# Kernel optimization log

Hardware: AMD Instinct MI355X
Metric: run time of the kernel (lower is better)

Reference implementation:

```python
import jax, jax.numpy as jnp
import numpy as np

B, S, D, DFF = 4, 2048, 1024, 4096


def setup_inputs() -> dict:
    key = jax.random.key(0)
    ks = jax.random.split(key, 7)
    scale = 1.0 / np.sqrt(D)
    return {
        "x": jax.random.normal(ks[0], (B, S, D), dtype=jnp.float32),
        "wq": jax.random.normal(ks[1], (D, D), dtype=jnp.float32) * scale,
        "wk": jax.random.normal(ks[2], (D, D), dtype=jnp.float32) * scale,
        "wv": jax.random.normal(ks[3], (D, D), dtype=jnp.float32) * scale,
        "wo": jax.random.normal(ks[4], (D, D), dtype=jnp.float32) * scale,
        "w1": jax.random.normal(ks[5], (D, DFF), dtype=jnp.float32) * scale,
        "w2": jax.random.normal(ks[6], (DFF, D), dtype=jnp.float32) * (1.0 / np.sqrt(DFF)),
    }


def reference(x, wq, wk, wv, wo, w1, w2):
    # Single-head attention, NO 1/sqrt(d) scaling (faithful to source).
    q = x @ wq  # [B,S,D]
    k = x @ wk
    v = x @ wv
    scores = jnp.einsum("bsd,btd->bst", q, k)  # [B,S,S]
    weights = jax.nn.softmax(scores, axis=-1)
    attn = jnp.einsum("bst,btd->bsd", weights, v)
    proj = attn @ wo
    hidden = jax.nn.relu(proj @ w1)  # [B,S,DFF]
    out = hidden @ w2
    return out + x
```

## Files before the change

### kernel.cpp

```cpp
#include <hip/hip_runtime.h>
#include <hip/hip_bf16.h>
#include <hip/hip_fp16.h>


typedef _Float16 f16;
typedef __attribute__((ext_vector_type(8))) _Float16 f16x8;
typedef __attribute__((ext_vector_type(4))) _Float16 f16x4;
typedef __attribute__((ext_vector_type(4))) float f32x4;

#define BM 128
#define BN 128
#define BK 64

__device__ inline void gload16(const void* g, void* l) {
    __builtin_amdgcn_global_load_lds(
        (const __attribute__((address_space(1))) void*)g,
        (__attribute__((address_space(3))) void*)l, 16, 0, 0);
}

template<int EPI>
__global__ __launch_bounds__(256, 2)
void gemm_f16(const f16* __restrict__ A, const f16* __restrict__ Bt,
              const float* __restrict__ Res, void* __restrict__ Cv,
              int K, int lda, int ldb, int ldc,
              long long sA, long long sB, long long sC)
{
    __shared__ char smem[32 * 1024];
    f16* Ash = (f16*)smem;
    f16* Bsh = (f16*)(smem + 16384);
    float* xbuf = (float*)smem;

    const int t = threadIdx.x;
    const int z = blockIdx.z;
    A  += (size_t)z * sA;
    Bt += (size_t)z * sB;

    const int bm0 = blockIdx.x * BM;
    const int bn0 = blockIdx.y * BN;

    const int lane = t & 63;
    const int wid  = t >> 6;
    const int quad = lane >> 4;
    const int m16  = lane & 15;
    const int ks   = wid & 1;
    const int wn64 = (wid >> 1) * 64;

    const int r0 = t >> 3;
    const int kc = ((t & 7) ^ (r0 & 7)) * 8;
    const char* gA[4]; const char* gB[4];
    #pragma unroll
    for (int i = 0; i < 4; ++i) {
        gA[i] = (const char*)(A  + (size_t)(bm0 + i * 32 + r0) * lda + kc);
        gB[i] = (const char*)(Bt + (size_t)(bn0 + i * 32 + r0) * ldb + kc);
    }
    char* lA = (char*)Ash + (wid << 10);
    char* lB = (char*)Bsh + (wid << 10);

    f32x4 acc[8][4] = {};

    const int nk = K / BK;
    #define ISSUE(kt) do { const int ko = (kt) * 128;   \
        gload16(gA[0] + ko, lA);                        \
        gload16(gA[1] + ko, lA + 4096);                 \
        gload16(gA[2] + ko, lA + 8192);                 \
        gload16(gA[3] + ko, lA + 12288);                \
        gload16(gB[0] + ko, lB);                        \
        gload16(gB[1] + ko, lB + 4096);                 \
        gload16(gB[2] + ko, lB + 8192);                 \
        gload16(gB[3] + ko, lB + 12288); } while (0)

    const int swz = m16 & 7;
    const int ha  = ((ks * 4 + quad) ^ swz) * 8;

    ISSUE(0);
    for (int kt = 0; kt < nk; ++kt) {
        __syncthreads();
        f16x8 af[8], bf[4];
        #pragma unroll
        for (int i = 0; i < 8; ++i)
            af[i] = *(const f16x8*)&Ash[(i * 16 + m16) * BK + ha];
        #pragma unroll
        for (int j = 0; j < 4; ++j)
            bf[j] = *(const f16x8*)&Bsh[(wn64 + j * 16 + m16) * BK + ha];
        __syncthreads();
        if (kt + 1 < nk) ISSUE(kt + 1);
        #pragma unroll
        for (int i = 0; i < 8; ++i)
            #pragma unroll
            for (int j = 0; j < 4; ++j)
                acc[i][j] = __builtin_amdgcn_mfma_f32_16x16x32_f16(
                                af[i], bf[j], acc[i][j], 0, 0, 0);
    }
    #undef ISSUE

    float* xb = xbuf + (wid >> 1) * 4096;
    #define XIDX(row, col) ((row) * 64 + ((col) ^ (((row) & 4) << 2)))
    if (ks == 1) {
        #pragma unroll
        for (int i = 0; i < 4; ++i)
            #pragma unroll
            for (int j = 0; j < 4; ++j)
                #pragma unroll
                for (int ri = 0; ri < 4; ++ri)
                    xb[XIDX(i * 16 + quad * 4 + ri, j * 16 + m16)] = acc[i][j][ri];
    }
    __syncthreads();
    if (ks == 0) {
        #pragma unroll
        for (int i = 0; i < 4; ++i)
            #pragma unroll
            for (int j = 0; j < 4; ++j)
                #pragma unroll
                for (int ri = 0; ri < 4; ++ri)
                    acc[i][j][ri] += xb[XIDX(i * 16 + quad * 4 + ri, j * 16 + m16)];
    }
    __syncthreads();
    if (ks == 0) {
        #pragma unroll
        for (int i = 0; i < 4; ++i)
            #pragma unroll
            for (int j = 0; j < 4; ++j)
                #pragma unroll
                for (int ri = 0; ri < 4; ++ri)
                    xb[XIDX(i * 16 + quad * 4 + ri, j * 16 + m16)] = acc[i + 4][j][ri];
    }
    __syncthreads();
    if (ks == 1) {
        #pragma unroll
        for (int i = 0; i < 4; ++i)
            #pragma unroll
            for (int j = 0; j < 4; ++j)
                #pragma unroll
                for (int ri = 0; ri < 4; ++ri)
                    acc[i + 4][j][ri] += xb[XIDX(i * 16 + quad * 4 + ri, j * 16 + m16)];
    }
    #undef XIDX

    #define STORE_TILE(IB, RB)                                                  \
        do {                                                                    \
            if (EPI <= 1) {                                                     \
                f16* C = (f16*)Cv + (size_t)z * sC;                             \
                _Pragma("unroll")                                               \
                for (int i = 0; i < 4; ++i)                                     \
                    _Pragma("unroll")                                           \
                    for (int ri = 0; ri < 4; ++ri) {                            \
                        const size_t row = (size_t)(bm0 + (RB) + i * 16 + quad * 4 + ri); \
                        f16* cp = C + row * ldc + (bn0 + wn64 + m16);           \
                        _Pragma("unroll")                                       \
                        for (int j = 0; j < 4; ++j) {                           \
                            float v = acc[(IB) + i][j][ri];                     \
                            if (EPI == 1) v = fmaxf(v, 0.0f);                   \
                            cp[j * 16] = (f16)v;                                \
                        }                                                       \
                    }                                                           \
            } else {                                                            \
                float* C = (float*)Cv + (size_t)z * sC;                         \
                _Pragma("unroll")                                               \
                for (int i = 0; i < 4; ++i)                                     \
                    _Pragma("unroll")                                           \
                    for (int ri = 0; ri < 4; ++ri) {                            \
                        const size_t row = (size_t)(bm0 + (RB) + i * 16 + quad * 4 + ri); \
                        float* cp = C + row * ldc + (bn0 + wn64 + m16);         \
                        const float* rp = (EPI == 3)                            \
                            ? Res + row * ldc + (bn0 + wn64 + m16) : nullptr;   \
                        _Pragma("unroll")                                       \
                        for (int j = 0; j < 4; ++j) {                           \
                            float v = acc[(IB) + i][j][ri];                     \
                            if (EPI == 3) v += rp[j * 16];                      \
                            cp[j * 16] = v;                                     \
                        }                                                       \
                    }                                                           \
            }                                                                   \
        } while (0)

    if (ks == 0) STORE_TILE(0, 0);
    else         STORE_TILE(4, 64);
    #undef STORE_TILE
}

template<int EPI>
__global__ __launch_bounds__(256, 2)
void gemm_ns(const f16* __restrict__ A, const f16* __restrict__ Bt,
             void* __restrict__ Cv,
             int K, int lda, int ldb, int ldc)
{
    __shared__ f16 Ash[BM * BK];
    __shared__ f16 Bsh[BN * BK];

    const int t = threadIdx.x;
    const int bm0 = blockIdx.x * BM;
    const int bn0 = blockIdx.y * BN;

    const int lane = t & 63;
    const int wid  = t >> 6;
    const int quad = lane >> 4;
    const int m16  = lane & 15;
    const int wm = (wid & 1) * 64;
    const int wn = (wid >> 1) * 64;

    const int r0 = t >> 3;
    const int kc = ((t & 7) ^ (r0 & 7)) * 8;
    const char* gA[4]; const char* gB[4];
    #pragma unroll
    for (int i = 0; i < 4; ++i) {
        gA[i] = (const char*)(A  + (size_t)(bm0 + i * 32 + r0) * lda + kc);
        gB[i] = (const char*)(Bt + (size_t)(bn0 + i * 32 + r0) * ldb + kc);
    }
    char* lA = (char*)Ash + (wid << 10);
    char* lB = (char*)Bsh + (wid << 10);

    f32x4 acc[4][4] = {};

    const int nk = K / BK;
    #define ISSUE(kt) do { const int ko = (kt) * 128;   \
        gload16(gA[0] + ko, lA);                        \
        gload16(gA[1] + ko, lA + 4096);                 \
        gload16(gA[2] + ko, lA + 8192);                 \
        gload16(gA[3] + ko, lA + 12288);                \
        gload16(gB[0] + ko, lB);                        \
        gload16(gB[1] + ko, lB + 4096);                 \
        gload16(gB[2] + ko, lB + 8192);                 \
        gload16(gB[3] + ko, lB + 12288); } while (0)

    const int swz = m16 & 7;

    ISSUE(0);
    for (int kt = 0; kt < nk; ++kt) {
        __syncthreads();
        f16x8 af[2][4], bf[2][4];
        #pragma unroll
        for (int s = 0; s < 2; ++s) {
            const int ha = (((s << 2) | quad) ^ swz) * 8;
            #pragma unroll
            for (int i = 0; i < 4; ++i) {
                af[s][i] = *(const f16x8*)&Ash[(wm + i * 16 + m16) * BK + ha];
                bf[s][i] = *(const f16x8*)&Bsh[(wn + i * 16 + m16) * BK + ha];
            }
        }
        __syncthreads();
        if (kt + 1 < nk) ISSUE(kt + 1);
        #pragma unroll
        for (int s = 0; s < 2; ++s)
            #pragma unroll
            for (int i = 0; i < 4; ++i)
                #pragma unroll
                for (int j = 0; j < 4; ++j)
                    acc[i][j] = __builtin_amdgcn_mfma_f32_16x16x32_f16(
                                    af[s][i], bf[s][j], acc[i][j], 0, 0, 0);
    }
    #undef ISSUE

    f16* C = (f16*)Cv;
    #pragma unroll
    for (int i = 0; i < 4; ++i)
        #pragma unroll
        for (int ri = 0; ri < 4; ++ri) {
            const size_t row = (size_t)(bm0 + wm + i * 16 + quad * 4 + ri);
            f16* cp = C + row * ldc + (bn0 + wn + m16);
            #pragma unroll
            for (int j = 0; j < 4; ++j) {
                float v = acc[i][j][ri];
                if (EPI == 1) v = fmaxf(v, 0.0f);
                cp[j * 16] = (f16)v;
            }
        }
}

__global__ __launch_bounds__(256, 2)
void gemm_dd(const f16* __restrict__ A0, const f16* __restrict__ B0, f16* __restrict__ C0,
             const f16* __restrict__ A1, const f16* __restrict__ B1, f16* __restrict__ C1)
{
    const int LD = 1024;
    __shared__ char smem[32 * 1024];
    f16* Ash = (f16*)smem;
    f16* Bsh = (f16*)(smem + 16384);
    float* xred = (float*)smem;

    const int t = threadIdx.x;
    const int z = blockIdx.z;
    const f16* A = z ? A1 : A0;
    const f16* B = z ? B1 : B0;
    f16* C = z ? C1 : C0;

    const int bm0 = blockIdx.x * 64;
    const int bn0 = blockIdx.y * 64;

    const int lane = t & 63;
    const int wid  = t >> 6;
    const int quad = lane >> 4;
    const int m16  = lane & 15;

    const int rr = t >> 4;
    const int kc = ((t & 15) ^ (rr & 15)) * 8;
    const char* gA[4]; const char* gB[4];
    #pragma unroll
    for (int i = 0; i < 4; ++i) {
        gA[i] = (const char*)(A + (size_t)(bm0 + i * 16 + rr) * LD + kc);
        gB[i] = (const char*)(B + (size_t)(bn0 + i * 16 + rr) * LD + kc);
    }
    char* lA = (char*)Ash + (wid << 10);
    char* lB = (char*)Bsh + (wid << 10);

    f32x4 acc[4][4] = {};

    #define ISSUE(kt) do { const int ko = (kt) * 256;   \
        gload16(gA[0] + ko, lA);                        \
        gload16(gA[1] + ko, lA + 4096);                 \
        gload16(gA[2] + ko, lA + 8192);                 \
        gload16(gA[3] + ko, lA + 12288);                \
        gload16(gB[0] + ko, lB);                        \
        gload16(gB[1] + ko, lB + 4096);                 \
        gload16(gB[2] + ko, lB + 8192);                 \
        gload16(gB[3] + ko, lB + 12288); } while (0)

    const int sl = ((wid * 4 + quad) ^ m16) * 8;

    ISSUE(0);
    for (int kt = 0; kt < 8; ++kt) {
        __syncthreads();
        f16x8 af[4], bf[4];
        #pragma unroll
        for (int i = 0; i < 4; ++i) {
            af[i] = *(const f16x8*)&Ash[(i * 16 + m16) * 128 + sl];
            bf[i] = *(const f16x8*)&Bsh[(i * 16 + m16) * 128 + sl];
        }
        __syncthreads();
        if (kt + 1 < 8) ISSUE(kt + 1);
        #pragma unroll
        for (int i = 0; i < 4; ++i)
            #pragma unroll
            for (int j = 0; j < 4; ++j)
                acc[i][j] = __builtin_amdgcn_mfma_f32_16x16x32_f16(
                                af[i], bf[j], acc[i][j], 0, 0, 0);
    }
    #undef ISSUE

    #define XIDX(row, col) ((row) * 64 + ((col) ^ (((row) & 4) << 2)))
    #define WR(base) do {                                                       \
        _Pragma("unroll")                                                       \
        for (int i = 0; i < 4; ++i)                                             \
            _Pragma("unroll")                                                   \
            for (int j = 0; j < 4; ++j)                                         \
                _Pragma("unroll")                                               \
                for (int ri = 0; ri < 4; ++ri)                                  \
                    (base)[XIDX(i * 16 + quad * 4 + ri, j * 16 + m16)] = acc[i][j][ri]; \
        } while (0)
    #define RD(base) do {                                                       \
        _Pragma("unroll")                                                       \
        for (int i = 0; i < 4; ++i)                                             \
            _Pragma("unroll")                                                   \
            for (int j = 0; j < 4; ++j)                                         \
                _Pragma("unroll")                                               \
                for (int ri = 0; ri < 4; ++ri)                                  \
                    acc[i][j][ri] += (base)[XIDX(i * 16 + quad * 4 + ri, j * 16 + m16)]; \
        } while (0)

    __syncthreads();
    if (wid == 2) WR(xred);
    if (wid == 3) WR(xred + 4096);
    __syncthreads();
    if (wid == 0) RD(xred);
    if (wid == 1) RD(xred + 4096);
    __syncthreads();
    if (wid == 1) WR(xred);
    __syncthreads();
    if (wid == 0) {
        RD(xred);
        #pragma unroll
        for (int i = 0; i < 4; ++i)
            #pragma unroll
            for (int ri = 0; ri < 4; ++ri) {
                const size_t row = (size_t)(bm0 + i * 16 + quad * 4 + ri);
                f16* cp = C + row * LD + (bn0 + m16);
                #pragma unroll
                for (int j = 0; j < 4; ++j)
                    cp[j * 16] = (f16)acc[i][j][ri];
            }
    }
    #undef WR
    #undef RD
    #undef XIDX
}

__global__ __launch_bounds__(256)
void transpose_cast(const float* __restrict__ in, f16* __restrict__ out,
                    int R, int C)
{
    __shared__ float tile[64][65];
    const int c0 = blockIdx.x * 64, r0 = blockIdx.y * 64;
    const int tc = threadIdx.x & 63, tr = threadIdx.x >> 6;
    #pragma unroll
    for (int i = 0; i < 16; ++i)
        tile[tr + i * 4][tc] = in[(size_t)(r0 + tr + i * 4) * C + c0 + tc];
    __syncthreads();
    #pragma unroll
    for (int i = 0; i < 16; ++i)
        out[(size_t)(c0 + tr + i * 4) * R + r0 + tc] = (f16)tile[tc][tr + i * 4];
}

__global__ __launch_bounds__(256)
void cast_f16(const float* __restrict__ in, f16* __restrict__ out)
{
    const size_t i = ((size_t)blockIdx.x * 256 + threadIdx.x) * 4;
    float4 v = *(const float4*)(in + i);
    f16x4 o; o.x = (f16)v.x; o.y = (f16)v.y; o.z = (f16)v.z; o.w = (f16)v.w;
    *(f16x4*)(out + i) = o;
}

__global__ __launch_bounds__(256)
void cast3_f16(const float* __restrict__ s0, const float* __restrict__ s1,
               const float* __restrict__ s2,
               f16* __restrict__ d0, f16* __restrict__ d1, f16* __restrict__ d2)
{
    const int z = blockIdx.z;
    const float* in = (z == 0) ? s0 : (z == 1) ? s1 : s2;
    f16* out = (z == 0) ? d0 : (z == 1) ? d1 : d2;
    const size_t i = ((size_t)blockIdx.x * 256 + threadIdx.x) * 4;
    float4 v = *(const float4*)(in + i);
    f16x4 o; o.x = (f16)v.x; o.y = (f16)v.y; o.z = (f16)v.z; o.w = (f16)v.w;
    *(f16x4*)(out + i) = o;
}

__global__ __launch_bounds__(256)
void softmax_f16(float* __restrict__ S)
{
    __shared__ float red[256];
    float* p = S + (size_t)blockIdx.x * 2048;
    f16* q = (f16*)p;
    const int t = threadIdx.x;

    float4 u0 = *(const float4*)(p + t * 4);
    float4 u1 = *(const float4*)(p + 1024 + t * 4);

    float m = fmaxf(fmaxf(fmaxf(u0.x, u0.y), fmaxf(u0.z, u0.w)),
                    fmaxf(fmaxf(u1.x, u1.y), fmaxf(u1.z, u1.w)));
    red[t] = m;
    __syncthreads();
    #pragma unroll
    for (int s = 128; s > 0; s >>= 1) {
        if (t < s) red[t] = fmaxf(red[t], red[t + s]);
        __syncthreads();
    }
    const float rowmax = red[0];
    __syncthreads();

    u0.x = __expf(u0.x - rowmax); u0.y = __expf(u0.y - rowmax);
    u0.z = __expf(u0.z - rowmax); u0.w = __expf(u0.w - rowmax);
    u1.x = __expf(u1.x - rowmax); u1.y = __expf(u1.y - rowmax);
    u1.z = __expf(u1.z - rowmax); u1.w = __expf(u1.w - rowmax);

    red[t] = (u0.x + u0.y + u0.z + u0.w) + (u1.x + u1.y + u1.z + u1.w);
    __syncthreads();
    #pragma unroll
    for (int s = 128; s > 0; s >>= 1) {
        if (t < s) red[t] += red[t + s];
        __syncthreads();
    }
    const float inv = 1.0f / red[0];
    __syncthreads();

    f16x4 o0, o1;
    o0.x = (f16)(u0.x * inv); o0.y = (f16)(u0.y * inv);
    o0.z = (f16)(u0.z * inv); o0.w = (f16)(u0.w * inv);
    o1.x = (f16)(u1.x * inv); o1.y = (f16)(u1.y * inv);
    o1.z = (f16)(u1.z * inv); o1.w = (f16)(u1.w * inv);
    *(f16x4*)(q + t * 4)        = o0;
    *(f16x4*)(q + 1024 + t * 4) = o1;
}

extern "C" void kernel_launch(void* const* d_in, const int* in_sizes, int n_in,
                              void* d_out, int out_size, void* d_ws, size_t ws_size,
                              hipStream_t stream)
{
    const float* x  = (const float*)d_in[0];
    const float* wq = (const float*)d_in[1];
    const float* wk = (const float*)d_in[2];
    const float* wv = (const float*)d_in[3];
    const float* wo = (const float*)d_in[4];
    const float* w1 = (const float*)d_in[5];
    const float* w2 = (const float*)d_in[6];
    float* out = (float*)d_out;

    const int S = 2048, D = 1024, DFF = 4096, Bb = 4;
    const int NTOK = Bb * S;
    const size_t M1 = 1024 * 1024;

    f16* W    = (f16*)d_ws;
    f16* xh   = W;
    f16* wqh  = W + 8 * M1;
    f16* wkh  = W + 9 * M1;
    f16* wvh  = W + 10 * M1;
    f16* woT  = W + 11 * M1;
    f16* w1T  = W + 12 * M1;
    f16* w2T  = W + 16 * M1;
    f16* wqkT = W + 20 * M1;
    f16* wvoT = W + 21 * M1;
    f16* qp   = W + 22 * M1;
    f16* vwT  = W + 30 * M1;
    float* sb = (float*)(W + 38 * M1);
    f16* ph   = (f16*)sb;
    f16* pj   = xh;
    f16* hd   = qp;

    dim3 blk(256);

    cast_f16<<<dim3(NTOK * D / 1024), blk, 0, stream>>>(x, xh);
    cast3_f16<<<dim3(D * D / 1024, 1, 3), blk, 0, stream>>>(
        wq, wk, wv, wqh, wkh, wvh);
    transpose_cast<<<dim3(D / 64, D / 64), blk, 0, stream>>>(wo, woT, D, D);
    transpose_cast<<<dim3(DFF / 64, D / 64), blk, 0, stream>>>(w1, w1T, D, DFF);
    transpose_cast<<<dim3(D / 64, DFF / 64), blk, 0, stream>>>(w2, w2T, DFF, D);
    gemm_dd<<<dim3(16, 16, 2), blk, 0, stream>>>(
        wkh, wqh, wqkT, woT, wvh, wvoT);

    gemm_f16<0><<<dim3(NTOK / BM, D / BN, 1), blk, 0, stream>>>(
        xh, wqkT, nullptr, qp, D, D, D, D, 0, 0, 0);
    gemm_f16<0><<<dim3(D / BM, NTOK / BN, 1), blk, 0, stream>>>(
        wvoT, xh, nullptr, vwT, D, D, D, NTOK, 0, 0, 0);

    gemm_f16<2><<<dim3(S / BM, S / BN, Bb), blk, 0, stream>>>(
        qp, xh, nullptr, sb, D, D, D, S,
        (long long)S * D, (long long)S * D, (long long)S * S);

    softmax_f16<<<dim3(NTOK), blk, 0, stream>>>(sb);

    gemm_f16<0><<<dim3(S / BM, D / BN, Bb), blk, 0, stream>>>(
        ph, vwT, nullptr, pj, S, 4096, NTOK, D,
        (long long)S * 4096, (long long)S, (long long)S * D);

    gemm_ns<1><<<dim3(NTOK / BM, DFF / BN, 1), blk, 0, stream>>>(
        pj, w1T, hd, D, D, D, DFF);

    gemm_f16<3><<<dim3(NTOK / BM, D / BN, 1), blk, 0, stream>>>(
        hd, w2T, x, out, DFF, DFF, DFF, D, 0, 0, 0);
}
```

Before: 417.4 us.

## Use 256x256-tile 8-wave pipelined GEMM for the FFN up-projection

```diff
diff --git a/kernel.cpp b/kernel.cpp
--- a/kernel.cpp
+++ b/kernel.cpp
@@ -266,6 +266,147 @@
         }
 }
 
+template<int EPI>
+__global__ __launch_bounds__(512, 2)
+void gemm_8p(const f16* __restrict__ A, const f16* __restrict__ Bt,
+             void* __restrict__ Cv, int K, int lda, int ldb, int ldc)
+{
+    extern __shared__ char smem[];
+
+    const int t = threadIdx.x;
+    const int bm0 = blockIdx.x * 256;
+    const int bn0 = blockIdx.y * 256;
+
+    const int lane = t & 63;
+    const int wid  = t >> 6;
+    const int quad = lane >> 4;
+    const int m16  = lane & 15;
+    const int wm   = (wid >> 2) * 128;
+    const int wn   = (wid & 3) * 64;
+
+    const int sr = t >> 3;
+    const int jp = ((t & 7) ^ (sr & 7)) * 8;
+    const char* gA = (const char*)(A  + (size_t)(bm0 + sr) * lda + jp);
+    const char* gB = (const char*)(Bt + (size_t)(bn0 + sr) * ldb + jp);
+    char* lAd = smem + wid * 1024;
+    char* lBd = smem + 65536 + wid * 1024;
+
+    const int aoff = (wm + m16) * 128;
+    const int boff = (wn + m16) * 128;
+    const int swz0 = ((quad)     ^ (m16 & 7)) * 16;
+    const int swz1 = ((4 | quad) ^ (m16 & 7)) * 16;
+
+    f32x4 acc[8][4] = {};
+    f16x8 af[4][2];
+    f16x8 bf[2][2][2];
+
+    const int nt = K / 64;
+
+    #define STAGE_A(TT, BI, H) do {                                          \
+        const char* s_ = gA + ((size_t)((H) * 128) * lda + (size_t)(TT) * 64) * 2; \
+        char* d_ = lAd + (BI) * 32768 + (H) * 16384;                         \
+        gload16(s_, d_);                                                     \
+        gload16(s_ + (size_t)64 * lda * 2, d_ + 8192); } while (0)
+    #define STAGE_B(TT, BI, H) do {                                          \
+        const char* s_ = gB + ((size_t)((H) * 128) * ldb + (size_t)(TT) * 64) * 2; \
+        char* d_ = lBd + (BI) * 32768 + (H) * 16384;                         \
+        gload16(s_, d_);                                                     \
+        gload16(s_ + (size_t)64 * ldb * 2, d_ + 8192); } while (0)
+    #define LOAD_A4(BI, BASE) do {                                           \
+        _Pragma("unroll")                                                    \
+        for (int i_ = 0; i_ < 4; ++i_) {                                     \
+            af[i_][0] = *(const f16x8*)(smem + (BI) * 32768 + aoff + ((BASE) + i_) * 2048 + swz0); \
+            af[i_][1] = *(const f16x8*)(smem + (BI) * 32768 + aoff + ((BASE) + i_) * 2048 + swz1); } } while (0)
+    #define LOAD_B2(BI, G) do {                                              \
+        _Pragma("unroll")                                                    \
+        for (int j_ = 0; j_ < 2; ++j_) {                                     \
+            bf[G][j_][0] = *(const f16x8*)(smem + 65536 + (BI) * 32768 + boff + ((G) * 2 + j_) * 2048 + swz0); \
+            bf[G][j_][1] = *(const f16x8*)(smem + 65536 + (BI) * 32768 + boff + ((G) * 2 + j_) * 2048 + swz1); } } while (0)
+    #define MFMA_Q(MH, NG) do {                                              \
+        _Pragma("unroll")                                                    \
+        for (int s_ = 0; s_ < 2; ++s_)                                       \
+            _Pragma("unroll")                                                \
+            for (int i_ = 0; i_ < 4; ++i_)                                   \
+                _Pragma("unroll")                                            \
+                for (int j_ = 0; j_ < 2; ++j_)                               \
+                    acc[(MH) * 4 + i_][(NG) * 2 + j_] =                      \
+                        __builtin_amdgcn_mfma_f32_16x16x32_f16(              \
+                            af[i_][s_], bf[NG][j_][s_],                      \
+                            acc[(MH) * 4 + i_][(NG) * 2 + j_], 0, 0, 0); } while (0)
+    #define PHASE_TAIL(MH, NG) do {                                          \
+        __builtin_amdgcn_s_barrier();                                        \
+        asm volatile("s_waitcnt lgkmcnt(0)" ::: "memory");                   \
+        __builtin_amdgcn_sched_barrier(0);                                   \
+        __builtin_amdgcn_s_setprio(1);                                       \
+        MFMA_Q(MH, NG);                                                      \
+        __builtin_amdgcn_s_setprio(0);                                       \
+        __builtin_amdgcn_s_barrier(); } while (0)
+
+    STAGE_B(0, 0, 0); STAGE_B(0, 0, 1);
+    STAGE_A(0, 0, 0); STAGE_A(0, 0, 1);
+    if (nt > 1) {
+        STAGE_B(1, 1, 0); STAGE_B(1, 1, 1);
+        asm volatile("s_waitcnt vmcnt(4)" ::: "memory");
+    } else {
+        asm volatile("s_waitcnt vmcnt(0)" ::: "memory");
+    }
+    __builtin_amdgcn_sched_barrier(0);
+    __builtin_amdgcn_s_barrier();
+
+    #define TILE4(TT, BI) do {                                               \
+                                                                     \
+        if ((TT) > 0) {                                                      \
+            if ((TT) + 1 < nt) asm volatile("s_waitcnt vmcnt(4)" ::: "memory"); \
+            else               asm volatile("s_waitcnt vmcnt(0)" ::: "memory"); \
+            __builtin_amdgcn_sched_barrier(0);                               \
+        }                                                                    \
+        LOAD_A4(BI, 0);                                                      \
+        LOAD_B2(BI, 0);                                                      \
+        if ((TT) + 1 < nt) STAGE_A((TT) + 1, (BI) ^ 1, 0);                   \
+        PHASE_TAIL(0, 0);                                                    \
+                                                                     \
+        LOAD_B2(BI, 1);                                                      \
+        if ((TT) + 1 < nt) STAGE_A((TT) + 1, (BI) ^ 1, 1);                   \
+        PHASE_TAIL(0, 1);                                                    \
+                                                                     \
+        LOAD_A4(BI, 4);                                                      \
+        if ((TT) + 2 < nt) STAGE_B((TT) + 2, BI, 0);                         \
+        PHASE_TAIL(1, 0);                                                    \
+                                                                     \
+        if ((TT) + 2 < nt) STAGE_B((TT) + 2, BI, 1);                         \
+        PHASE_TAIL(1, 1);                                                    \
+    } while (0)
+
+    #pragma unroll 1
+    for (int tt = 0; tt < nt; tt += 2) {
+        TILE4(tt, 0);
+        TILE4(tt + 1, 1);
+    }
+
+    #undef TILE4
+    #undef PHASE_TAIL
+    #undef MFMA_Q
+    #undef LOAD_B2
+    #undef LOAD_A4
+    #undef STAGE_B
+    #undef STAGE_A
+
+    f16* C = (f16*)Cv;
+    #pragma unroll
+    for (int i = 0; i < 8; ++i)
+        #pragma unroll
+        for (int ri = 0; ri < 4; ++ri) {
+            const size_t row = (size_t)(bm0 + wm + i * 16 + quad * 4 + ri);
+            f16* cp = C + row * ldc + (bn0 + wn + m16);
+            #pragma unroll
+            for (int j = 0; j < 4; ++j) {
+                float v = acc[i][j][ri];
+                if (EPI == 1) v = fmaxf(v, 0.0f);
+                cp[j * 16] = (f16)v;
+            }
+        }
+}
+
 __global__ __launch_bounds__(256, 2)
 void gemm_dd(const f16* __restrict__ A0, const f16* __restrict__ B0, f16* __restrict__ C0,
              const f16* __restrict__ A1, const f16* __restrict__ B1, f16* __restrict__ C1)
@@ -528,7 +669,7 @@
         ph, vwT, nullptr, pj, S, 4096, NTOK, D,
         (long long)S * 4096, (long long)S, (long long)S * D);
 
-    gemm_ns<1><<<dim3(NTOK / BM, DFF / BN, 1), blk, 0, stream>>>(
+    gemm_8p<1><<<dim3(NTOK / 256, DFF / 256), dim3(512), 131072, stream>>>(
         pj, w1T, hd, D, D, D, DFF);
 
     gemm_f16<3><<<dim3(NTOK / BM, D / BN, 1), blk, 0, stream>>>(
```

After: 432.7 us. +3.7%, slower.
